# Kernel tuning notes

Hardware: AMD Instinct MI355X
Metric: run time of the kernel (lower is better)

Reference implementation:

```python
import jax, jax.numpy as jnp
import numpy as np

N_NODES = 100000
N_EDGES = 1600000
D = 64
K1 = 10   # conv1 hops
K2 = 3    # stacked conv hops


def _gcn_norm(edge_index, num_nodes, dtype):
    # PyG gcn_norm with add_self_loops=False: sym normalization D^-1/2 A D^-1/2
    row, col = edge_index[0], edge_index[1]
    deg = jax.ops.segment_sum(jnp.ones(row.shape, dtype), col, num_segments=num_nodes)
    dinv = jnp.where(deg > 0, jax.lax.rsqrt(jnp.maximum(deg, 1.0)), 0.0)
    return dinv[row] * dinv[col]  # [E]


def _tagconv(x, ws, b, row, col, nrm, num_nodes):
    # out = sum_k (A_hat^k x) @ W_k + b ; ws: [K+1, D, D]
    out = x @ ws[0]
    h = x
    for k in range(1, ws.shape[0]):
        msg = h[row] * nrm[:, None]                       # [E, D] gather
        h = jax.ops.segment_sum(msg, col, num_segments=num_nodes)  # [N, D] scatter-add
        out = out + h @ ws[k]
    return out + b


def setup_inputs() -> dict:
    key = jax.random.key(0)
    ks = jax.random.split(key, 8)
    x = jax.random.normal(ks[0], (N_NODES, D), dtype=jnp.float32)
    edge_index = jax.random.randint(ks[1], (2, N_EDGES), 0, N_NODES, dtype=jnp.int64)
    s = 1.0 / np.sqrt(D)
    w1 = jax.random.normal(ks[2], (K1 + 1, D, D), dtype=jnp.float32) * s
    b1 = jnp.zeros((D,), dtype=jnp.float32)
    w2 = jax.random.normal(ks[3], (K2 + 1, D, D), dtype=jnp.float32) * s
    b2 = jnp.zeros((D,), dtype=jnp.float32)
    wc = jax.random.normal(ks[4], (D, D), dtype=jnp.float32) * s
    bc = jnp.zeros((D,), dtype=jnp.float32)
    return {"x": x, "edge_index": edge_index, "w1": w1, "b1": b1,
            "w2": w2, "b2": b2, "wc": wc, "bc": bc}


def reference(x, edge_index, w1, b1, w2, b2, wc, bc):
    num_nodes = x.shape[0]
    row, col = edge_index[0], edge_index[1]
    nrm = _gcn_norm(edge_index, num_nodes, x.dtype)
    h = jnp.tanh(_tagconv(x, w1, b1, row, col, nrm, num_nodes))
    h = jnp.tanh(_tagconv(h, w2, b2, row, col, nrm, num_nodes))
    return h @ wc + bc
```

## Files before the change

kernel.cpp:

```cpp
#include <hip/hip_runtime.h>
#include <hip/hip_bf16.h>

#define PAD 16
#define NBKT_MAX 512

typedef __attribute__((ext_vector_type(8))) short short8;
typedef __attribute__((ext_vector_type(4))) float float4v;

__device__ __forceinline__ short8 as_s8(uint4 v) {
    union { uint4 u; short8 s; } x; x.u = v; return x.s;
}

__device__ __forceinline__ int pad_up(int v) { return (v + (PAD - 1)) & ~(PAD - 1); }


__global__ __launch_bounds__(256) void hist_kernel(const int* __restrict__ col,
                                                   int* __restrict__ blockHist, int E, int nbkt) {
    __shared__ int h[NBKT_MAX];
    for (int i = threadIdx.x; i < nbkt; i += 256) h[i] = 0;
    __syncthreads();
    int chunk = (E + gridDim.x - 1) / gridDim.x;
    int lo = blockIdx.x * chunk, hi = min(lo + chunk, E);
    for (int e = lo + threadIdx.x; e < hi; e += 256) atomicAdd(&h[col[e] >> 9], 1);
    __syncthreads();
    for (int i = threadIdx.x; i < nbkt; i += 256) blockHist[i * 256 + blockIdx.x] = h[i];
}

__global__ __launch_bounds__(256) void bscan_kernel(int* __restrict__ blockHist,
                                                    int* __restrict__ bktTot, int nbkt) {
    __shared__ int a[256], b[256];
    int bkt = blockIdx.x;
    int t = threadIdx.x;
    int v = blockHist[bkt * 256 + t];
    a[t] = v;
    __syncthreads();
    int* s = a; int* d = b;
    for (int off = 1; off < 256; off <<= 1) {
        int x = s[t];
        if (t >= off) x += s[t - off];
        d[t] = x;
        __syncthreads();
        int* tmp = s; s = d; d = tmp;
    }
    blockHist[bkt * 256 + t] = s[t] - v;
    if (t == 255) bktTot[bkt] = s[t];
}

__global__ void scan_small(const int* __restrict__ in, int* __restrict__ outp, int n) {
    __shared__ int a[256], b[256];
    int t = threadIdx.x;
    int v = t < n ? in[t] : 0;
    a[t] = v;
    __syncthreads();
    int* s = a; int* d = b;
    for (int off = 1; off < 256; off <<= 1) {
        int x = s[t];
        if (t >= off) x += s[t - off];
        d[t] = x;
        __syncthreads();
        int* tmp = s; s = d; d = tmp;
    }
    if (t < n) outp[t] = s[t] - v;
}

__global__ __launch_bounds__(256) void scatter_kernel(const int* __restrict__ row,
                                                      const int* __restrict__ col,
                                                      const int* __restrict__ blockHist,
                                                      const int* __restrict__ bktOff,
                                                      int2* __restrict__ pairs, int E, int nbkt) {
    __shared__ int cur[NBKT_MAX];
    for (int i = threadIdx.x; i < nbkt; i += 256)
        cur[i] = bktOff[i] + blockHist[i * 256 + blockIdx.x];
    __syncthreads();
    int chunk = (E + gridDim.x - 1) / gridDim.x;
    int lo = blockIdx.x * chunk, hi = min(lo + chunk, E);
    for (int e = lo + threadIdx.x; e < hi; e += 256) {
        int dn = col[e];
        int p = atomicAdd(&cur[dn >> 9], 1);
        pairs[p] = make_int2(row[e], dn);
    }
}

__global__ __launch_bounds__(256) void deg_pairs_kernel(
        const int2* __restrict__ pairs, const int* __restrict__ bktOff,
        const int* __restrict__ bktTot,
        int* __restrict__ deg, float* __restrict__ dinv, float* __restrict__ dinv2,
        float* __restrict__ sdeg, int N) {
    __shared__ int cnt[512];
    int b = blockIdx.x, d0 = b << 9;
    for (int i = threadIdx.x; i < 512; i += 256) cnt[i] = 0;
    __syncthreads();
    int lo = bktOff[b], hi = lo + bktTot[b];
    for (int p = lo + threadIdx.x; p < hi; p += 256)
        atomicAdd(&cnt[pairs[p].y - d0], 1);
    __syncthreads();
    for (int i = threadIdx.x; i < 512; i += 256) {
        int d = d0 + i;
        if (d < N) {
            int c = cnt[i];
            deg[d] = c;
            float v = c > 0 ? rsqrtf((float)c) : 0.0f;
            dinv[d] = v;
            dinv2[d] = v * v;
            sdeg[d] = c > 0 ? sqrtf((float)c) : 0.0f;
        }
    }
}

__global__ void scan_phaseA(const int* __restrict__ deg, int* __restrict__ chunkSum, int N) {
    int t = threadIdx.x;
    int idx = blockIdx.x * 512 + t;
    int v = idx < N ? pad_up(deg[idx]) : 0;
    for (int o = 32; o > 0; o >>= 1) v += __shfl_down(v, o, 64);
    __shared__ int wsum[8];
    if ((t & 63) == 0) wsum[t >> 6] = v;
    __syncthreads();
    if (t == 0) {
        int s = 0;
        for (int i = 0; i < 8; ++i) s += wsum[i];
        chunkSum[blockIdx.x] = s;
    }
}

__global__ void scan_phaseC(const int* __restrict__ deg, const int* __restrict__ chunkOff,
                            int* __restrict__ rowptr, int N) {
    __shared__ int a[512], b[512];
    int t = threadIdx.x;
    int idx = blockIdx.x * 512 + t;
    int v = idx < N ? pad_up(deg[idx]) : 0;
    a[t] = v;
    __syncthreads();
    int* s = a; int* d = b;
    for (int off = 1; off < 512; off <<= 1) {
        int x = s[t];
        if (t >= off) x += s[t - off];
        d[t] = x;
        __syncthreads();
        int* tmp = s; s = d; d = tmp;
    }
    if (idx < N) rowptr[idx] = chunkOff[blockIdx.x] + s[t] - v;
    if (idx == N - 1) rowptr[N] = chunkOff[blockIdx.x] + s[t];
}

__global__ __launch_bounds__(256) void cluster_kernel(const int2* __restrict__ pairs,
                                                      const int* __restrict__ bktOff,
                                                      const int* __restrict__ bktTot,
                                                      const int* __restrict__ rowptr,
                                                      int* __restrict__ srcs, int N) {
    __shared__ int cur[512];
    int b = blockIdx.x;
    int d0 = b << 9;
    for (int i = threadIdx.x; i < 512; i += 256) {
        int d = d0 + i;
        cur[i] = (d < N) ? rowptr[d] : 0;
    }
    __syncthreads();
    int lo = bktOff[b], hi = lo + bktTot[b];
    for (int p = lo + threadIdx.x; p < hi; p += 256) {
        int2 e = pairs[p];
        int pos = atomicAdd(&cur[e.y - d0], 1);
        srcs[pos] = e.x;
    }
    __syncthreads();
    for (int i = threadIdx.x; i < 512; i += 256) {
        int d = d0 + i;
        if (d < N) {
            int p = cur[i];
            int p1 = rowptr[d + 1];
            for (; p < p1; ++p) srcs[p] = N;
        }
    }
}


__global__ void wcvt_kernel(const float* __restrict__ w1, const float* __restrict__ w2,
                            const float* __restrict__ wc, __hip_bfloat16* __restrict__ wf) {
    int idx = blockIdx.x * blockDim.x + threadIdx.x;
    if (idx >= 16 * 4096) return;
    int g = idx >> 12, r = idx & 4095;
    int j = r & 7, lane = (r >> 3) & 63, u = (r >> 9) & 3, t = r >> 11;
    int k = t * 32 + (lane >> 4) * 8 + j;
    int n = u * 16 + (lane & 15);
    const float* W = (g < 11) ? (w1 + (size_t)g * 4096)
                  : (g < 15) ? (w2 + (size_t)(g - 11) * 4096) : wc;
    wf[idx] = __float2bfloat16(W[k * 64 + n]);
}

__global__ void zero_pads_kernel(__hip_bfloat16* __restrict__ gbase, size_t gstride,
                                 int nbuf, int N) {
    int i = blockIdx.x * blockDim.x + threadIdx.x;
    int b = i >> 6;
    if (b < nbuf) gbase[(size_t)b * gstride + (size_t)N * 64 + (i & 63)] = __float2bfloat16(0.0f);
}

__global__ void cvt_g_kernel(const float* __restrict__ x, const float* __restrict__ dinv,
                             __hip_bfloat16* __restrict__ g, int N) {
    int i = blockIdx.x * blockDim.x + threadIdx.x;
    if (i < N * 64) g[i] = __float2bfloat16(dinv[i >> 6] * x[i]);
}


__global__ __launch_bounds__(256) void hop_kernel(
        const __hip_bfloat16* __restrict__ g_in,
        const int* __restrict__ srcs, const int* __restrict__ rowptr,
        const float* __restrict__ dinv2,
        __hip_bfloat16* __restrict__ g_out, int n) {
    const int lane = threadIdx.x & 63;
    const int quad = lane >> 4;
    const int c4 = lane & 15;
    int gw = __builtin_amdgcn_readfirstlane((blockIdx.x * blockDim.x + threadIdx.x) >> 6);
    int nw = (gridDim.x * blockDim.x) >> 6;
    for (int d = gw; d < n; d += nw) {
        int p0 = rowptr[d], p1 = rowptr[d + 1];
        float a0 = 0.f, a1 = 0.f, a2 = 0.f, a3 = 0.f;
        for (int p = p0; p < p1; p += 16) {
            int4 sq = ((const int4*)(srcs + p))[quad];
            const uint2* r0 = (const uint2*)(g_in + (size_t)sq.x * 64);
            const uint2* r1 = (const uint2*)(g_in + (size_t)sq.y * 64);
            const uint2* r2 = (const uint2*)(g_in + (size_t)sq.z * 64);
            const uint2* r3 = (const uint2*)(g_in + (size_t)sq.w * 64);
            uint2 v0 = r0[c4], v1 = r1[c4], v2 = r2[c4], v3 = r3[c4];
            a0 += __uint_as_float(v0.x << 16); a1 += __uint_as_float(v0.x & 0xffff0000u);
            a2 += __uint_as_float(v0.y << 16); a3 += __uint_as_float(v0.y & 0xffff0000u);
            a0 += __uint_as_float(v1.x << 16); a1 += __uint_as_float(v1.x & 0xffff0000u);
            a2 += __uint_as_float(v1.y << 16); a3 += __uint_as_float(v1.y & 0xffff0000u);
            a0 += __uint_as_float(v2.x << 16); a1 += __uint_as_float(v2.x & 0xffff0000u);
            a2 += __uint_as_float(v2.y << 16); a3 += __uint_as_float(v2.y & 0xffff0000u);
            a0 += __uint_as_float(v3.x << 16); a1 += __uint_as_float(v3.x & 0xffff0000u);
            a2 += __uint_as_float(v3.y << 16); a3 += __uint_as_float(v3.y & 0xffff0000u);
        }
        a0 += __shfl_xor(a0, 16); a1 += __shfl_xor(a1, 16);
        a2 += __shfl_xor(a2, 16); a3 += __shfl_xor(a3, 16);
        a0 += __shfl_xor(a0, 32); a1 += __shfl_xor(a1, 32);
        a2 += __shfl_xor(a2, 32); a3 += __shfl_xor(a3, 32);
        if (quad == 0) {
            float s = dinv2[d];
            union { __hip_bfloat16 h[4]; uint2 u; } pk;
            pk.h[0] = __float2bfloat16(s * a0);
            pk.h[1] = __float2bfloat16(s * a1);
            pk.h[2] = __float2bfloat16(s * a2);
            pk.h[3] = __float2bfloat16(s * a3);
            ((uint2*)(g_out + (size_t)d * 64))[c4] = pk.u;
        }
    }
}


template<int NG>
__global__ __launch_bounds__(256) void final_kernel(
        const __hip_bfloat16* gbase, size_t gstride,
        const __hip_bfloat16* __restrict__ wf,
        const float* __restrict__ sdeg, const float* __restrict__ bias,
        const float* __restrict__ scale,
        __hip_bfloat16* out16, int ntiles) {
    const int lane = threadIdx.x & 63;
    const int col = lane & 15, quad = lane >> 4;
    int wv = (blockIdx.x * blockDim.x + threadIdx.x) >> 6;
    int nwv = (gridDim.x * blockDim.x) >> 6;
    const uint4* wfq = (const uint4*)wf;
    for (int tile = wv; tile < ntiles; tile += nwv) {
        int base = tile * 16;
        float4v acc0 = {0.f, 0.f, 0.f, 0.f};
        float4v acc1 = {0.f, 0.f, 0.f, 0.f};
        float4v acc2 = {0.f, 0.f, 0.f, 0.f};
        float4v acc3 = {0.f, 0.f, 0.f, 0.f};
#pragma unroll
        for (int g = 0; g < NG; ++g) {
            const uint4* ga = (const uint4*)(gbase + (size_t)g * gstride);
            const uint4* wg = wfq + (size_t)g * 512;
#pragma unroll
            for (int t = 0; t < 2; ++t) {
                short8 a = as_s8(ga[(size_t)(base + col) * 8 + t * 4 + quad]);
                short8 b0 = as_s8(wg[(t * 4 + 0) * 64 + lane]);
                short8 b1 = as_s8(wg[(t * 4 + 1) * 64 + lane]);
                short8 b2 = as_s8(wg[(t * 4 + 2) * 64 + lane]);
                short8 b3 = as_s8(wg[(t * 4 + 3) * 64 + lane]);
                acc0 = __builtin_amdgcn_mfma_f32_16x16x32_bf16(a, b0, acc0, 0, 0, 0);
                acc1 = __builtin_amdgcn_mfma_f32_16x16x32_bf16(a, b1, acc1, 0, 0, 0);
                acc2 = __builtin_amdgcn_mfma_f32_16x16x32_bf16(a, b2, acc2, 0, 0, 0);
                acc3 = __builtin_amdgcn_mfma_f32_16x16x32_bf16(a, b3, acc3, 0, 0, 0);
            }
        }
#pragma unroll
        for (int r = 0; r < 4; ++r) {
            int nd = base + quad * 4 + r;
            float sd = sdeg[nd];
            float sc = scale ? scale[nd] : 1.0f;
            float f0 = sc * tanhf(sd * acc0[r] + bias[0 * 16 + col]);
            float f1 = sc * tanhf(sd * acc1[r] + bias[1 * 16 + col]);
            float f2 = sc * tanhf(sd * acc2[r] + bias[2 * 16 + col]);
            float f3 = sc * tanhf(sd * acc3[r] + bias[3 * 16 + col]);
            out16[(size_t)nd * 64 + 0 * 16 + col] = __float2bfloat16(f0);
            out16[(size_t)nd * 64 + 1 * 16 + col] = __float2bfloat16(f1);
            out16[(size_t)nd * 64 + 2 * 16 + col] = __float2bfloat16(f2);
            out16[(size_t)nd * 64 + 3 * 16 + col] = __float2bfloat16(f3);
        }
    }
}


__global__ __launch_bounds__(256) void head_kernel(
        const __hip_bfloat16* __restrict__ v16, const __hip_bfloat16* __restrict__ wfc,
        const float* __restrict__ bc, float* __restrict__ out, int ntiles) {
    const int lane = threadIdx.x & 63;
    const int col = lane & 15, quad = lane >> 4;
    int wv = (blockIdx.x * blockDim.x + threadIdx.x) >> 6;
    int nwv = (gridDim.x * blockDim.x) >> 6;
    const uint4* va = (const uint4*)v16;
    const uint4* wg = (const uint4*)wfc;
    for (int tile = wv; tile < ntiles; tile += nwv) {
        int base = tile * 16;
        float4v acc0 = {0.f, 0.f, 0.f, 0.f};
        float4v acc1 = {0.f, 0.f, 0.f, 0.f};
        float4v acc2 = {0.f, 0.f, 0.f, 0.f};
        float4v acc3 = {0.f, 0.f, 0.f, 0.f};
#pragma unroll
        for (int t = 0; t < 2; ++t) {
            short8 a = as_s8(va[(size_t)(base + col) * 8 + t * 4 + quad]);
            short8 b0 = as_s8(wg[(t * 4 + 0) * 64 + lane]);
            short8 b1 = as_s8(wg[(t * 4 + 1) * 64 + lane]);
            short8 b2 = as_s8(wg[(t * 4 + 2) * 64 + lane]);
            short8 b3 = as_s8(wg[(t * 4 + 3) * 64 + lane]);
            acc0 = __builtin_amdgcn_mfma_f32_16x16x32_bf16(a, b0, acc0, 0, 0, 0);
            acc1 = __builtin_amdgcn_mfma_f32_16x16x32_bf16(a, b1, acc1, 0, 0, 0);
            acc2 = __builtin_amdgcn_mfma_f32_16x16x32_bf16(a, b2, acc2, 0, 0, 0);
            acc3 = __builtin_amdgcn_mfma_f32_16x16x32_bf16(a, b3, acc3, 0, 0, 0);
        }
#pragma unroll
        for (int r = 0; r < 4; ++r) {
            int nd = base + quad * 4 + r;
            out[(size_t)nd * 64 + 0 * 16 + col] = acc0[r] + bc[0 * 16 + col];
            out[(size_t)nd * 64 + 1 * 16 + col] = acc1[r] + bc[1 * 16 + col];
            out[(size_t)nd * 64 + 2 * 16 + col] = acc2[r] + bc[2 * 16 + col];
            out[(size_t)nd * 64 + 3 * 16 + col] = acc3[r] + bc[3 * 16 + col];
        }
    }
}


extern "C" void kernel_launch(void* const* d_in, const int* in_sizes, int n_in,
                              void* d_out, int out_size, void* d_ws, size_t ws_size,
                              hipStream_t stream) {
    const float* x  = (const float*)d_in[0];
    const int*   ei = (const int*)d_in[1];
    const float* w1 = (const float*)d_in[2];
    const float* b1 = (const float*)d_in[3];
    const float* w2 = (const float*)d_in[4];
    const float* b2 = (const float*)d_in[5];
    const float* wc = (const float*)d_in[6];
    const float* bc = (const float*)d_in[7];
    float* out = (float*)d_out;

    const int N = in_sizes[0] / 64;
    const int E = in_sizes[1] / 2;
    const int K1 = 10, K2 = 3;
    const int* row = ei;
    const int* col = ei + E;
    const int Epad = E + (PAD - 1) * N + 64;
    const int NBUF = 11;
    const int nbkt = (N + 511) >> 9;
    const size_t gstride = (((size_t)(N + 1) * 64) + 127) & ~(size_t)127;

    char* base = (char*)d_ws;
    auto alloc = [&](size_t bytes) { void* p = (void*)base; base += (bytes + 255) & ~(size_t)255; return p; };
    int*   deg      = (int*)alloc((size_t)N * 4);
    int*   rowptr   = (int*)alloc((size_t)(N + 1) * 4);
    int*   chunkSum = (int*)alloc(256 * 4);
    int*   chunkOff = (int*)alloc(256 * 4);
    int*   blockHist= (int*)alloc((size_t)NBKT_MAX * 256 * 4);
    int*   bktTot   = (int*)alloc((size_t)NBKT_MAX * 4);
    int*   bktOff   = (int*)alloc((size_t)NBKT_MAX * 4);
    float* dinv     = (float*)alloc((size_t)N * 4);
    float* dinv2    = (float*)alloc((size_t)N * 4);
    float* sdeg     = (float*)alloc((size_t)N * 4);
    int*   srcs     = (int*)alloc((size_t)Epad * 4);
    __hip_bfloat16* wf    = (__hip_bfloat16*)alloc((size_t)16 * 4096 * 2);
    __hip_bfloat16* gbase = (__hip_bfloat16*)alloc((size_t)NBUF * gstride * 2);

    auto G = [&](int k) { return gbase + (size_t)k * gstride; };
    int2* pairs = (int2*)G(9);
    __hip_bfloat16* vbuf16 = G(5);

    const int numChunks = (N + 511) / 512;
    const int xBlocks = (N * 64 + 255) / 256;
    const int gBlocks = 2048;
    const int ntiles = (N + 15) / 16;

    hist_kernel<<<256, 256, 0, stream>>>(col, blockHist, E, nbkt);
    bscan_kernel<<<nbkt, 256, 0, stream>>>(blockHist, bktTot, nbkt);
    scan_small<<<1, 256, 0, stream>>>(bktTot, bktOff, nbkt);
    scatter_kernel<<<256, 256, 0, stream>>>(row, col, blockHist, bktOff, pairs, E, nbkt);
    deg_pairs_kernel<<<nbkt, 256, 0, stream>>>(pairs, bktOff, bktTot, deg, dinv, dinv2, sdeg, N);
    scan_phaseA<<<numChunks, 512, 0, stream>>>(deg, chunkSum, N);
    scan_small<<<1, 256, 0, stream>>>(chunkSum, chunkOff, numChunks);
    scan_phaseC<<<numChunks, 512, 0, stream>>>(deg, chunkOff, rowptr, N);
    cluster_kernel<<<nbkt, 256, 0, stream>>>(pairs, bktOff, bktTot, rowptr, srcs, N);

    wcvt_kernel<<<(16 * 4096 + 255) / 256, 256, 0, stream>>>(w1, w2, wc, wf);
    zero_pads_kernel<<<(NBUF * 64 + 255) / 256, 256, 0, stream>>>(gbase, gstride, NBUF, N);
    cvt_g_kernel<<<xBlocks, 256, 0, stream>>>(x, dinv, G(0), N);

    for (int k = 1; k <= K1; ++k)
        hop_kernel<<<gBlocks, 256, 0, stream>>>(G(k - 1), srcs, rowptr, dinv2, G(k), N);

    final_kernel<11><<<gBlocks, 256, 0, stream>>>(gbase, gstride, wf, sdeg, b1, dinv,
                                                  G(1), ntiles);

    for (int k = 1; k <= K2; ++k)
        hop_kernel<<<gBlocks, 256, 0, stream>>>(G(k), srcs, rowptr, dinv2, G(k + 1), N);

    final_kernel<4><<<gBlocks, 256, 0, stream>>>(G(1), gstride, wf + (size_t)11 * 4096,
                                                 sdeg, b2, nullptr, vbuf16, ntiles);

    head_kernel<<<gBlocks, 256, 0, stream>>>(vbuf16, wf + (size_t)15 * 4096, bc, out, ntiles);
}
```

Before: 669.3 us.

## Pack edge pairs, vectorize preprocessing, fuse degree scan, and tile final kernel by four

Several separate changes. The hist and scatter kernels now read col and row as int4 with a grid-stride loop. Edge pairs are packed into a single 32-bit word (source shifted left by 9, plus the low 9 bits of the destination), which halves the traffic through the pairs buffer. The degree kernel is fused with scan phase A, and the hop and MFMA kernels use nontemporal loads. The final kernel now processes four 16-row tiles per wave so the weight fragments are reused, with launch bounds and grid sizes adjusted to match. The packing assumes the row index fits in 23 bits, and the quad tiling raises register pressure.

```diff
diff --git a/kernel.cpp b/kernel.cpp
--- a/kernel.cpp
+++ b/kernel.cpp
@@ -6,9 +6,10 @@
 
 typedef __attribute__((ext_vector_type(8))) short short8;
 typedef __attribute__((ext_vector_type(4))) float float4v;
-
-__device__ __forceinline__ short8 as_s8(uint4 v) {
-    union { uint4 u; short8 s; } x; x.u = v; return x.s;
+typedef unsigned int __attribute__((ext_vector_type(4))) uint4v;
+
+__device__ __forceinline__ short8 s8(uint4v v) {
+    union { uint4v u; short8 s; } x; x.u = v; return x.s;
 }
 
 __device__ __forceinline__ int pad_up(int v) { return (v + (PAD - 1)) & ~(PAD - 1); }
@@ -19,9 +20,17 @@
     __shared__ int h[NBKT_MAX];
     for (int i = threadIdx.x; i < nbkt; i += 256) h[i] = 0;
     __syncthreads();
-    int chunk = (E + gridDim.x - 1) / gridDim.x;
-    int lo = blockIdx.x * chunk, hi = min(lo + chunk, E);
-    for (int e = lo + threadIdx.x; e < hi; e += 256) atomicAdd(&h[col[e] >> 9], 1);
+    int E4 = E >> 2;
+    int stride = gridDim.x * 256;
+    for (int i = blockIdx.x * 256 + threadIdx.x; i < E4; i += stride) {
+        int4 c = ((const int4*)col)[i];
+        atomicAdd(&h[c.x >> 9], 1);
+        atomicAdd(&h[c.y >> 9], 1);
+        atomicAdd(&h[c.z >> 9], 1);
+        atomicAdd(&h[c.w >> 9], 1);
+    }
+    if (blockIdx.x == 0)
+        for (int e = E4 * 4 + threadIdx.x; e < E; e += 256) atomicAdd(&h[col[e] >> 9], 1);
     __syncthreads();
     for (int i = threadIdx.x; i < nbkt; i += 256) blockHist[i * 256 + blockIdx.x] = h[i];
 }
@@ -67,37 +76,55 @@
                                                       const int* __restrict__ col,
                                                       const int* __restrict__ blockHist,
                                                       const int* __restrict__ bktOff,
-                                                      int2* __restrict__ pairs, int E, int nbkt) {
+                                                      unsigned int* __restrict__ pairs,
+                                                      int E, int nbkt) {
     __shared__ int cur[NBKT_MAX];
     for (int i = threadIdx.x; i < nbkt; i += 256)
         cur[i] = bktOff[i] + blockHist[i * 256 + blockIdx.x];
     __syncthreads();
-    int chunk = (E + gridDim.x - 1) / gridDim.x;
-    int lo = blockIdx.x * chunk, hi = min(lo + chunk, E);
-    for (int e = lo + threadIdx.x; e < hi; e += 256) {
-        int dn = col[e];
-        int p = atomicAdd(&cur[dn >> 9], 1);
-        pairs[p] = make_int2(row[e], dn);
-    }
-}
-
-__global__ __launch_bounds__(256) void deg_pairs_kernel(
-        const int2* __restrict__ pairs, const int* __restrict__ bktOff,
+    int E4 = E >> 2;
+    int stride = gridDim.x * 256;
+    for (int i = blockIdx.x * 256 + threadIdx.x; i < E4; i += stride) {
+        int4 c = ((const int4*)col)[i];
+        int4 r = ((const int4*)row)[i];
+        int p0 = atomicAdd(&cur[c.x >> 9], 1);
+        pairs[p0] = ((unsigned int)r.x << 9) | (unsigned int)(c.x & 511);
+        int p1 = atomicAdd(&cur[c.y >> 9], 1);
+        pairs[p1] = ((unsigned int)r.y << 9) | (unsigned int)(c.y & 511);
+        int p2 = atomicAdd(&cur[c.z >> 9], 1);
+        pairs[p2] = ((unsigned int)r.z << 9) | (unsigned int)(c.z & 511);
+        int p3 = atomicAdd(&cur[c.w >> 9], 1);
+        pairs[p3] = ((unsigned int)r.w << 9) | (unsigned int)(c.w & 511);
+    }
+    if (blockIdx.x == 0)
+        for (int e = E4 * 4 + threadIdx.x; e < E; e += 256) {
+            int dn = col[e];
+            int p = atomicAdd(&cur[dn >> 9], 1);
+            pairs[p] = ((unsigned int)row[e] << 9) | (unsigned int)(dn & 511);
+        }
+}
+
+__global__ __launch_bounds__(256) void deg_scanA_kernel(
+        const unsigned int* __restrict__ pairs, const int* __restrict__ bktOff,
         const int* __restrict__ bktTot,
         int* __restrict__ deg, float* __restrict__ dinv, float* __restrict__ dinv2,
-        float* __restrict__ sdeg, int N) {
+        float* __restrict__ sdeg, int* __restrict__ chunkSum, int N) {
     __shared__ int cnt[512];
+    __shared__ int wsum[4];
     int b = blockIdx.x, d0 = b << 9;
-    for (int i = threadIdx.x; i < 512; i += 256) cnt[i] = 0;
+    int t = threadIdx.x;
+    for (int i = t; i < 512; i += 256) cnt[i] = 0;
     __syncthreads();
     int lo = bktOff[b], hi = lo + bktTot[b];
-    for (int p = lo + threadIdx.x; p < hi; p += 256)
-        atomicAdd(&cnt[pairs[p].y - d0], 1);
-    __syncthreads();
-    for (int i = threadIdx.x; i < 512; i += 256) {
+    for (int p = lo + t; p < hi; p += 256)
+        atomicAdd(&cnt[pairs[p] & 511u], 1);
+    __syncthreads();
+    int sA = 0;
+    for (int i = t; i < 512; i += 256) {
+        int c = cnt[i];
+        sA += pad_up(c);
         int d = d0 + i;
         if (d < N) {
-            int c = cnt[i];
             deg[d] = c;
             float v = c > 0 ? rsqrtf((float)c) : 0.0f;
             dinv[d] = v;
@@ -105,21 +132,10 @@
             sdeg[d] = c > 0 ? sqrtf((float)c) : 0.0f;
         }
     }
-}
-
-__global__ void scan_phaseA(const int* __restrict__ deg, int* __restrict__ chunkSum, int N) {
-    int t = threadIdx.x;
-    int idx = blockIdx.x * 512 + t;
-    int v = idx < N ? pad_up(deg[idx]) : 0;
-    for (int o = 32; o > 0; o >>= 1) v += __shfl_down(v, o, 64);
-    __shared__ int wsum[8];
-    if ((t & 63) == 0) wsum[t >> 6] = v;
-    __syncthreads();
-    if (t == 0) {
-        int s = 0;
-        for (int i = 0; i < 8; ++i) s += wsum[i];
-        chunkSum[blockIdx.x] = s;
-    }
+    for (int o = 32; o > 0; o >>= 1) sA += __shfl_down(sA, o, 64);
+    if ((t & 63) == 0) wsum[t >> 6] = sA;
+    __syncthreads();
+    if (t == 0) chunkSum[b] = wsum[0] + wsum[1] + wsum[2] + wsum[3];
 }
 
 __global__ void scan_phaseC(const int* __restrict__ deg, const int* __restrict__ chunkOff,
@@ -142,7 +158,7 @@
     if (idx == N - 1) rowptr[N] = chunkOff[blockIdx.x] + s[t];
 }
 
-__global__ __launch_bounds__(256) void cluster_kernel(const int2* __restrict__ pairs,
+__global__ __launch_bounds__(256) void cluster_kernel(const unsigned int* __restrict__ pairs,
                                                       const int* __restrict__ bktOff,
                                                       const int* __restrict__ bktTot,
                                                       const int* __restrict__ rowptr,
@@ -157,9 +173,9 @@
     __syncthreads();
     int lo = bktOff[b], hi = lo + bktTot[b];
     for (int p = lo + threadIdx.x; p < hi; p += 256) {
-        int2 e = pairs[p];
-        int pos = atomicAdd(&cur[e.y - d0], 1);
-        srcs[pos] = e.x;
+        unsigned int e = pairs[p];
+        int pos = atomicAdd(&cur[e & 511u], 1);
+        srcs[pos] = (int)(e >> 9);
     }
     __syncthreads();
     for (int i = threadIdx.x; i < 512; i += 256) {
@@ -214,12 +230,15 @@
         int p0 = rowptr[d], p1 = rowptr[d + 1];
         float a0 = 0.f, a1 = 0.f, a2 = 0.f, a3 = 0.f;
         for (int p = p0; p < p1; p += 16) {
-            int4 sq = ((const int4*)(srcs + p))[quad];
-            const uint2* r0 = (const uint2*)(g_in + (size_t)sq.x * 64);
-            const uint2* r1 = (const uint2*)(g_in + (size_t)sq.y * 64);
-            const uint2* r2 = (const uint2*)(g_in + (size_t)sq.z * 64);
-            const uint2* r3 = (const uint2*)(g_in + (size_t)sq.w * 64);
-            uint2 v0 = r0[c4], v1 = r1[c4], v2 = r2[c4], v3 = r3[c4];
+            const unsigned long long* ps = (const unsigned long long*)(srcs + p);
+            unsigned long long s01 = __builtin_nontemporal_load(ps + quad * 2);
+            unsigned long long s23 = __builtin_nontemporal_load(ps + quad * 2 + 1);
+            int sx = (int)(s01 & 0xffffffffu), sy = (int)(s01 >> 32);
+            int sz = (int)(s23 & 0xffffffffu), sw = (int)(s23 >> 32);
+            uint2 v0 = ((const uint2*)(g_in + (size_t)sx * 64))[c4];
+            uint2 v1 = ((const uint2*)(g_in + (size_t)sy * 64))[c4];
+            uint2 v2 = ((const uint2*)(g_in + (size_t)sz * 64))[c4];
+            uint2 v3 = ((const uint2*)(g_in + (size_t)sw * 64))[c4];
             a0 += __uint_as_float(v0.x << 16); a1 += __uint_as_float(v0.x & 0xffff0000u);
             a2 += __uint_as_float(v0.y << 16); a3 += __uint_as_float(v0.y & 0xffff0000u);
             a0 += __uint_as_float(v1.x << 16); a1 += __uint_as_float(v1.x & 0xffff0000u);
@@ -247,7 +266,7 @@
 
 
 template<int NG>
-__global__ __launch_bounds__(256) void final_kernel(
+__global__ __launch_bounds__(256, 2) void final_kernel(
         const __hip_bfloat16* gbase, size_t gstride,
         const __hip_bfloat16* __restrict__ wf,
         const float* __restrict__ sdeg, const float* __restrict__ bias,
@@ -257,44 +276,74 @@
     const int col = lane & 15, quad = lane >> 4;
     int wv = (blockIdx.x * blockDim.x + threadIdx.x) >> 6;
     int nwv = (gridDim.x * blockDim.x) >> 6;
-    const uint4* wfq = (const uint4*)wf;
-    for (int tile = wv; tile < ntiles; tile += nwv) {
-        int base = tile * 16;
-        float4v acc0 = {0.f, 0.f, 0.f, 0.f};
-        float4v acc1 = {0.f, 0.f, 0.f, 0.f};
-        float4v acc2 = {0.f, 0.f, 0.f, 0.f};
-        float4v acc3 = {0.f, 0.f, 0.f, 0.f};
-#pragma unroll
+    const uint4v* wfq = (const uint4v*)wf;
+    int nquads = (ntiles + 3) >> 2;
+    for (int qd = wv; qd < nquads; qd += nwv) {
+        int t0 = qd * 4;
+        bool h1 = t0 + 1 < ntiles, h2 = t0 + 2 < ntiles, h3 = t0 + 3 < ntiles;
+        int bA = t0 * 16;
+        int bB = (h1 ? t0 + 1 : t0) * 16;
+        int bC = (h2 ? t0 + 2 : t0) * 16;
+        int bD = (h3 ? t0 + 3 : t0) * 16;
+        float4v aA0 = {0,0,0,0}, aA1 = {0,0,0,0}, aA2 = {0,0,0,0}, aA3 = {0,0,0,0};
+        float4v aB0 = {0,0,0,0}, aB1 = {0,0,0,0}, aB2 = {0,0,0,0}, aB3 = {0,0,0,0};
+        float4v aC0 = {0,0,0,0}, aC1 = {0,0,0,0}, aC2 = {0,0,0,0}, aC3 = {0,0,0,0};
+        float4v aD0 = {0,0,0,0}, aD1 = {0,0,0,0}, aD2 = {0,0,0,0}, aD3 = {0,0,0,0};
+#pragma unroll 1
         for (int g = 0; g < NG; ++g) {
-            const uint4* ga = (const uint4*)(gbase + (size_t)g * gstride);
-            const uint4* wg = wfq + (size_t)g * 512;
+            const uint4v* ga = (const uint4v*)(gbase + (size_t)g * gstride);
+            const uint4v* wg = wfq + (size_t)g * 512;
 #pragma unroll
             for (int t = 0; t < 2; ++t) {
-                short8 a = as_s8(ga[(size_t)(base + col) * 8 + t * 4 + quad]);
-                short8 b0 = as_s8(wg[(t * 4 + 0) * 64 + lane]);
-                short8 b1 = as_s8(wg[(t * 4 + 1) * 64 + lane]);
-                short8 b2 = as_s8(wg[(t * 4 + 2) * 64 + lane]);
-                short8 b3 = as_s8(wg[(t * 4 + 3) * 64 + lane]);
-                acc0 = __builtin_amdgcn_mfma_f32_16x16x32_bf16(a, b0, acc0, 0, 0, 0);
-                acc1 = __builtin_amdgcn_mfma_f32_16x16x32_bf16(a, b1, acc1, 0, 0, 0);
-                acc2 = __builtin_amdgcn_mfma_f32_16x16x32_bf16(a, b2, acc2, 0, 0, 0);
-                acc3 = __builtin_amdgcn_mfma_f32_16x16x32_bf16(a, b3, acc3, 0, 0, 0);
+                int fo = t * 4 + quad;
+                short8 fA = s8(__builtin_nontemporal_load(&ga[(size_t)(bA + col) * 8 + fo]));
+                short8 fB = s8(__builtin_nontemporal_load(&ga[(size_t)(bB + col) * 8 + fo]));
+                short8 fC = s8(__builtin_nontemporal_load(&ga[(size_t)(bC + col) * 8 + fo]));
+                short8 fD = s8(__builtin_nontemporal_load(&ga[(size_t)(bD + col) * 8 + fo]));
+                short8 w0 = s8(wg[(t * 4 + 0) * 64 + lane]);
+                short8 w1 = s8(wg[(t * 4 + 1) * 64 + lane]);
+                short8 w2 = s8(wg[(t * 4 + 2) * 64 + lane]);
+                short8 w3 = s8(wg[(t * 4 + 3) * 64 + lane]);
+                aA0 = __builtin_amdgcn_mfma_f32_16x16x32_bf16(fA, w0, aA0, 0, 0, 0);
+                aB0 = __builtin_amdgcn_mfma_f32_16x16x32_bf16(fB, w0, aB0, 0, 0, 0);
+                aC0 = __builtin_amdgcn_mfma_f32_16x16x32_bf16(fC, w0, aC0, 0, 0, 0);
+                aD0 = __builtin_amdgcn_mfma_f32_16x16x32_bf16(fD, w0, aD0, 0, 0, 0);
+                aA1 = __builtin_amdgcn_mfma_f32_16x16x32_bf16(fA, w1, aA1, 0, 0, 0);
+                aB1 = __builtin_amdgcn_mfma_f32_16x16x32_bf16(fB, w1, aB1, 0, 0, 0);
+                aC1 = __builtin_amdgcn_mfma_f32_16x16x32_bf16(fC, w1, aC1, 0, 0, 0);
+                aD1 = __builtin_amdgcn_mfma_f32_16x16x32_bf16(fD, w1, aD1, 0, 0, 0);
+                aA2 = __builtin_amdgcn_mfma_f32_16x16x32_bf16(fA, w2, aA2, 0, 0, 0);
+                aB2 = __builtin_amdgcn_mfma_f32_16x16x32_bf16(fB, w2, aB2, 0, 0, 0);
+                aC2 = __builtin_amdgcn_mfma_f32_16x16x32_bf16(fC, w2, aC2, 0, 0, 0);
+                aD2 = __builtin_amdgcn_mfma_f32_16x16x32_bf16(fD, w2, aD2, 0, 0, 0);
+                aA3 = __builtin_amdgcn_mfma_f32_16x16x32_bf16(fA, w3, aA3, 0, 0, 0);
+                aB3 = __builtin_amdgcn_mfma_f32_16x16x32_bf16(fB, w3, aB3, 0, 0, 0);
+                aC3 = __builtin_amdgcn_mfma_f32_16x16x32_bf16(fC, w3, aC3, 0, 0, 0);
+                aD3 = __builtin_amdgcn_mfma_f32_16x16x32_bf16(fD, w3, aD3, 0, 0, 0);
             }
         }
-#pragma unroll
-        for (int r = 0; r < 4; ++r) {
-            int nd = base + quad * 4 + r;
-            float sd = sdeg[nd];
-            float sc = scale ? scale[nd] : 1.0f;
-            float f0 = sc * tanhf(sd * acc0[r] + bias[0 * 16 + col]);
-            float f1 = sc * tanhf(sd * acc1[r] + bias[1 * 16 + col]);
-            float f2 = sc * tanhf(sd * acc2[r] + bias[2 * 16 + col]);
-            float f3 = sc * tanhf(sd * acc3[r] + bias[3 * 16 + col]);
-            out16[(size_t)nd * 64 + 0 * 16 + col] = __float2bfloat16(f0);
-            out16[(size_t)nd * 64 + 1 * 16 + col] = __float2bfloat16(f1);
-            out16[(size_t)nd * 64 + 2 * 16 + col] = __float2bfloat16(f2);
-            out16[(size_t)nd * 64 + 3 * 16 + col] = __float2bfloat16(f3);
-        }
+#define EPI(BASE, A0, A1, A2, A3)                                                    \
+        {                                                                            \
+            _Pragma("unroll")                                                        \
+            for (int r = 0; r < 4; ++r) {                                            \
+                int nd = (BASE) + quad * 4 + r;                                      \
+                float sd = sdeg[nd];                                                 \
+                float sc = scale ? scale[nd] : 1.0f;                                 \
+                float f0 = sc * tanhf(sd * (A0)[r] + bias[0 * 16 + col]);            \
+                float f1 = sc * tanhf(sd * (A1)[r] + bias[1 * 16 + col]);            \
+                float f2 = sc * tanhf(sd * (A2)[r] + bias[2 * 16 + col]);            \
+                float f3 = sc * tanhf(sd * (A3)[r] + bias[3 * 16 + col]);            \
+                out16[(size_t)nd * 64 + 0 * 16 + col] = __float2bfloat16(f0);        \
+                out16[(size_t)nd * 64 + 1 * 16 + col] = __float2bfloat16(f1);        \
+                out16[(size_t)nd * 64 + 2 * 16 + col] = __float2bfloat16(f2);        \
+                out16[(size_t)nd * 64 + 3 * 16 + col] = __float2bfloat16(f3);        \
+            }                                                                        \
+        }
+        EPI(bA, aA0, aA1, aA2, aA3)
+        if (h1) EPI(bB, aB0, aB1, aB2, aB3)
+        if (h2) EPI(bC, aC0, aC1, aC2, aC3)
+        if (h3) EPI(bD, aD0, aD1, aD2, aD3)
+#undef EPI
     }
 }
 
@@ -306,21 +355,18 @@
     const int col = lane & 15, quad = lane >> 4;
     int wv = (blockIdx.x * blockDim.x + threadIdx.x) >> 6;
     int nwv = (gridDim.x * blockDim.x) >> 6;
-    const uint4* va = (const uint4*)v16;
-    const uint4* wg = (const uint4*)wfc;
+    const uint4v* va = (const uint4v*)v16;
+    const uint4v* wg = (const uint4v*)wfc;
     for (int tile = wv; tile < ntiles; tile += nwv) {
         int base = tile * 16;
-        float4v acc0 = {0.f, 0.f, 0.f, 0.f};
-        float4v acc1 = {0.f, 0.f, 0.f, 0.f};
-        float4v acc2 = {0.f, 0.f, 0.f, 0.f};
-        float4v acc3 = {0.f, 0.f, 0.f, 0.f};
+        float4v acc0 = {0,0,0,0}, acc1 = {0,0,0,0}, acc2 = {0,0,0,0}, acc3 = {0,0,0,0};
 #pragma unroll
         for (int t = 0; t < 2; ++t) {
-            short8 a = as_s8(va[(size_t)(base + col) * 8 + t * 4 + quad]);
-            short8 b0 = as_s8(wg[(t * 4 + 0) * 64 + lane]);
-            short8 b1 = as_s8(wg[(t * 4 + 1) * 64 + lane]);
-            short8 b2 = as_s8(wg[(t * 4 + 2) * 64 + lane]);
-            short8 b3 = as_s8(wg[(t * 4 + 3) * 64 + lane]);
+            short8 a = s8(__builtin_nontemporal_load(&va[(size_t)(base + col) * 8 + t * 4 + quad]));
+            short8 b0 = s8(wg[(t * 4 + 0) * 64 + lane]);
+            short8 b1 = s8(wg[(t * 4 + 1) * 64 + lane]);
+            short8 b2 = s8(wg[(t * 4 + 2) * 64 + lane]);
+            short8 b3 = s8(wg[(t * 4 + 3) * 64 + lane]);
             acc0 = __builtin_amdgcn_mfma_f32_16x16x32_bf16(a, b0, acc0, 0, 0, 0);
             acc1 = __builtin_amdgcn_mfma_f32_16x16x32_bf16(a, b1, acc1, 0, 0, 0);
             acc2 = __builtin_amdgcn_mfma_f32_16x16x32_bf16(a, b2, acc2, 0, 0, 0);
@@ -378,20 +424,23 @@
     __hip_bfloat16* gbase = (__hip_bfloat16*)alloc((size_t)NBUF * gstride * 2);
 
     auto G = [&](int k) { return gbase + (size_t)k * gstride; };
-    int2* pairs = (int2*)G(9);
+    unsigned int* pairs = (unsigned int*)G(9);
     __hip_bfloat16* vbuf16 = G(5);
 
     const int numChunks = (N + 511) / 512;
     const int xBlocks = (N * 64 + 255) / 256;
     const int gBlocks = 2048;
     const int ntiles = (N + 15) / 16;
+    const int nquads = (ntiles + 3) / 4;
+    const int fBlocks = (nquads + 3) / 4;
+    const int hBlocks = (ntiles + 3) / 4;
 
     hist_kernel<<<256, 256, 0, stream>>>(col, blockHist, E, nbkt);
     bscan_kernel<<<nbkt, 256, 0, stream>>>(blockHist, bktTot, nbkt);
     scan_small<<<1, 256, 0, stream>>>(bktTot, bktOff, nbkt);
     scatter_kernel<<<256, 256, 0, stream>>>(row, col, blockHist, bktOff, pairs, E, nbkt);
-    deg_pairs_kernel<<<nbkt, 256, 0, stream>>>(pairs, bktOff, bktTot, deg, dinv, dinv2, sdeg, N);
-    scan_phaseA<<<numChunks, 512, 0, stream>>>(deg, chunkSum, N);
+    deg_scanA_kernel<<<nbkt, 256, 0, stream>>>(pairs, bktOff, bktTot, deg, dinv, dinv2,
+                                               sdeg, chunkSum, N);
     scan_small<<<1, 256, 0, stream>>>(chunkSum, chunkOff, numChunks);
     scan_phaseC<<<numChunks, 512, 0, stream>>>(deg, chunkOff, rowptr, N);
     cluster_kernel<<<nbkt, 256, 0, stream>>>(pairs, bktOff, bktTot, rowptr, srcs, N);
@@ -403,14 +452,14 @@
     for (int k = 1; k <= K1; ++k)
         hop_kernel<<<gBlocks, 256, 0, stream>>>(G(k - 1), srcs, rowptr, dinv2, G(k), N);
 
-    final_kernel<11><<<gBlocks, 256, 0, stream>>>(gbase, gstride, wf, sdeg, b1, dinv,
+    final_kernel<11><<<fBlocks, 256, 0, stream>>>(gbase, gstride, wf, sdeg, b1, dinv,
                                                   G(1), ntiles);
 
     for (int k = 1; k <= K2; ++k)
         hop_kernel<<<gBlocks, 256, 0, stream>>>(G(k), srcs, rowptr, dinv2, G(k + 1), N);
 
-    final_kernel<4><<<gBlocks, 256, 0, stream>>>(G(1), gstride, wf + (size_t)11 * 4096,
+    final_kernel<4><<<fBlocks, 256, 0, stream>>>(G(1), gstride, wf + (size_t)11 * 4096,
                                                  sdeg, b2, nullptr, vbuf16, ntiles);
 
-    head_kernel<<<gBlocks, 256, 0, stream>>>(vbuf16, wf + (size_t)15 * 4096, bc, out, ntiles);
-}
+    head_kernel<<<hBlocks, 256, 0, stream>>>(vbuf16, wf + (size_t)15 * 4096, bc, out, ntiles);
+}
```

Result: no change. 665.6 us (-0.5%).
